# Kernel tuning notes

Measured on AMD Instinct MI355X. Metric: run time of the kernel, lower is better.

The kernel has to match this reference:

```python
import jax, jax.numpy as jnp
import numpy as np
import math

EMBED_DIM = 1024
NUM_HEADS = 16
HEAD_DIM = EMBED_DIM // NUM_HEADS
INPUT_DIM = 1024


def setup_inputs() -> dict:
    key = jax.random.key(0)
    k_x, k_wqkv, k_wout = jax.random.split(key, 3)
    x = jax.random.normal(k_x, (4, 1, 2048, INPUT_DIM), dtype=jnp.float32)
    # xavier_uniform bounds
    def xavier(k, shape):
        fan_out, fan_in = shape
        bound = math.sqrt(6.0 / (fan_in + fan_out))
        return jax.random.uniform(k, shape, jnp.float32, -bound, bound)
    w_qkv = xavier(k_wqkv, (3 * EMBED_DIM, INPUT_DIM))
    b_qkv = jnp.zeros((3 * EMBED_DIM,), jnp.float32)
    w_out = xavier(k_wout, (EMBED_DIM, EMBED_DIM))
    b_out = jnp.zeros((EMBED_DIM,), jnp.float32)
    return {"x": x, "w_qkv": w_qkv, "b_qkv": b_qkv, "w_out": w_out, "b_out": b_out}


def reference(x, w_qkv, b_qkv, w_out, b_out):
    B, y, S, _ = x.shape  # y must be 1 (module reshape constraint)
    # QKV projection: [B, y, S, 3E]
    qkv = jnp.einsum('bysd,ed->byse', x, w_qkv) + b_qkv
    # reshape to [B, S, H, 3*head_dim] then [B, H, S, 3*head_dim]
    qkv = qkv.reshape(B, S, NUM_HEADS, 3 * HEAD_DIM).transpose(0, 2, 1, 3)
    q, k, v = jnp.split(qkv, 3, axis=-1)  # each [B, H, S, head_dim]
    logits = jnp.einsum('bhqd,bhkd->bhqk', q, k) / math.sqrt(HEAD_DIM)
    attn = jax.nn.softmax(logits, axis=-1)  # [B, H, S, S]
    vals = jnp.einsum('bhqk,bhkd->bhqd', attn, v)
    vals = vals.transpose(0, 2, 1, 3).reshape(B, S, EMBED_DIM)
    return jnp.einsum('bse,oe->bso', vals, w_out) + b_out  # [B, S, E]
```

## Files before the change

### kernel.cpp

```cpp
#include <hip/hip_runtime.h>

typedef __bf16 bf16;
typedef __bf16 bf16x8 __attribute__((ext_vector_type(8)));
typedef __bf16 bf16x4 __attribute__((ext_vector_type(4)));
typedef float f32x4 __attribute__((ext_vector_type(4)));
typedef float f32x16 __attribute__((ext_vector_type(16)));
typedef unsigned int u32x4 __attribute__((ext_vector_type(4)));

#define SM_SCALE 0.18033688011f

__device__ __forceinline__ f32x4 mfma16(bf16x8 a, bf16x8 b, f32x4 c) {
    return __builtin_amdgcn_mfma_f32_16x16x32_bf16(a, b, c, 0, 0, 0);
}
__device__ __forceinline__ f32x16 mfma32(bf16x8 a, bf16x8 b, f32x16 c) {
    return __builtin_amdgcn_mfma_f32_32x32x16_bf16(a, b, c, 0, 0, 0);
}

__device__ __forceinline__ void gload_lds16(const void* g, void* l) {
    __builtin_amdgcn_global_load_lds((const __attribute__((address_space(1))) void*)g,
                                     (__attribute__((address_space(3))) void*)l,
                                     16, 0, 0);
}

__device__ __forceinline__ unsigned cvtpk_bf16(float lo, float hi) {
    unsigned r;
    asm("v_cvt_pk_bf16_f32 %0, %1, %2" : "=v"(r) : "v"(lo), "v"(hi));
    return r;
}
__device__ __forceinline__ void plane32_swap(unsigned& a, unsigned& b) {
    asm("v_permlane32_swap_b32 %0, %1" : "+v"(a), "+v"(b));
}
__device__ __forceinline__ float vexp2(float x) {
    float r;
    asm("v_exp_f32 %0, %1" : "=v"(r) : "v"(x));
    return r;
}
__device__ __forceinline__ float vrcp(float x) {
    float r;
    asm("v_rcp_f32 %0, %1" : "=v"(r) : "v"(x));
    return r;
}

__device__ __forceinline__ void vpack_store(char* VwB, unsigned vwlow, bf16x8 v0, bf16x8 v1) {
    const u32x4 a = __builtin_bit_cast(u32x4, v0);
    const u32x4 b = __builtin_bit_cast(u32x4, v1);
#pragma unroll
    for (int j = 0; j < 8; ++j) {
        const unsigned sel = (j & 1) ? 0x07060302u : 0x05040100u;
        const unsigned w = __builtin_amdgcn_perm(b[j >> 1], a[j >> 1], sel);
        *(unsigned*)(VwB + j * 128 + (vwlow ^ (unsigned)(j << 4))) = w;
    }
}

__global__ void cvt_all(const float* __restrict__ x, const float* __restrict__ wq,
                        const float* __restrict__ wo, bf16* __restrict__ xb,
                        bf16* __restrict__ wqb, bf16* __restrict__ wob) {
    constexpr int NX = (8192 * 1024) / 4, NQ = (3072 * 1024) / 4, NO = (1024 * 1024) / 4;
    const int stride = gridDim.x * blockDim.x;
    for (int i = blockIdx.x * blockDim.x + threadIdx.x; i < NX + NQ + NO; i += stride) {
        const float* src;
        bf16* dst;
        int li;
        if (i < NX)           { src = x;  dst = xb;  li = i; }
        else if (i < NX + NQ) { src = wq; dst = wqb; li = i - NX; }
        else                  { src = wo; dst = wob; li = i - NX - NQ; }
        const f32x4 v = ((const f32x4*)src)[li];
        bf16x4 o;
#pragma unroll
        for (int j = 0; j < 4; ++j) o[j] = (bf16)v[j];
        ((bf16x4*)dst)[li] = o;
    }
}

#define G_STAGE(STBUF)                                                      \
    gload_lds16(apA,             ldsA + (STBUF) * 49152);                   \
    gload_lds16(apA +  8 * 1024, ldsA + (STBUF) * 49152 + 1024);            \
    gload_lds16(apA + 16 * 1024, ldsA + (STBUF) * 49152 + 2048);            \
    gload_lds16(apA + 24 * 1024, ldsA + (STBUF) * 49152 + 3072);            \
    gload_lds16(apB,             ldsB + (STBUF) * 49152);                   \
    gload_lds16(apB +  8 * 1024, ldsB + (STBUF) * 49152 + 1024);            \
    apA += 64; apB += 64;

#define G_TILE(BUF, VM, STBUF, DOSTAGE)                                     \
  {                                                                         \
    asm volatile("s_waitcnt vmcnt(" #VM ")" ::: "memory");                  \
    __builtin_amdgcn_s_barrier();                                           \
    bf16x8 a0[4], b0[4];                                                    \
    _Pragma("unroll") for (int mf = 0; mf < 4; ++mf)                        \
      a0[mf] = *(const bf16x8*)(baseAk0 + (BUF) * 49152 + mf * 2048);       \
    _Pragma("unroll") for (int nf = 0; nf < 4; ++nf)                        \
      b0[nf] = *(const bf16x8*)(baseBk0 + (BUF) * 49152 + nf * 2048);       \
    if (DOSTAGE) { G_STAGE(STBUF) }                                         \
    __builtin_amdgcn_s_setprio(1);                                          \
    _Pragma("unroll") for (int mf = 0; mf < 4; ++mf)                        \
      _Pragma("unroll") for (int nf = 0; nf < 4; ++nf)                      \
        acc[mf][nf] = mfma16(a0[mf], b0[nf], acc[mf][nf]);                  \
    __builtin_amdgcn_s_setprio(0);                                          \
    bf16x8 a1[4], b1[4];                                                    \
    _Pragma("unroll") for (int mf = 0; mf < 4; ++mf)                        \
      a1[mf] = *(const bf16x8*)(baseAk1 + (BUF) * 49152 + mf * 2048);       \
    _Pragma("unroll") for (int nf = 0; nf < 4; ++nf)                        \
      b1[nf] = *(const bf16x8*)(baseBk1 + (BUF) * 49152 + nf * 2048);       \
    __builtin_amdgcn_s_setprio(1);                                          \
    _Pragma("unroll") for (int mf = 0; mf < 4; ++mf)                        \
      _Pragma("unroll") for (int nf = 0; nf < 4; ++nf)                      \
        acc[mf][nf] = mfma16(a1[mf], b1[nf], acc[mf][nf]);                  \
    __builtin_amdgcn_s_setprio(0);                                          \
  }

template <typename OutT, bool QSCALE>
__global__ __launch_bounds__(512) void gemm256(const bf16* __restrict__ A,
                                               const bf16* __restrict__ Bw,
                                               const float* __restrict__ bias,
                                               OutT* __restrict__ C,
                                               int M, int N, int K) {
    __shared__ char lds[3 * 49152];
    const int tid = threadIdx.x;
    const int wave = tid >> 6, lane = tid & 63;
    const int ln15 = lane & 15, g4 = lane >> 4;
    const int wr = wave >> 1, wc = wave & 1;
    const int m0 = blockIdx.x * 256, n0 = blockIdx.y * 128;

    const int srow = lane >> 3;
    const int sgsw = ((lane & 7) ^ srow) * 8;
    const bf16* apA = A  + (size_t)(m0 + wave * 32 + srow) * K + sgsw;
    const bf16* apB = Bw + (size_t)(n0 + wave * 16 + srow) * K + sgsw;
    char* const ldsA = (char*)lds + wave * 4096;
    char* const ldsB = (char*)lds + 32768 + wave * 2048;

    const int cxor = ((g4 ^ (ln15 & 7)) << 4);
    const char* baseAk0 = (const char*)lds + (wr * 64 + ln15) * 128 + cxor;
    const char* baseAk1 = (const char*)lds + (((wr * 64 + ln15) * 128 + cxor) ^ 64);
    const char* baseBk0 = (const char*)lds + 32768 + (wc * 64 + ln15) * 128 + cxor;
    const char* baseBk1 = (const char*)lds + 32768 + (((wc * 64 + ln15) * 128 + cxor) ^ 64);

    f32x4 acc[4][4] = {};

    G_STAGE(0)
    G_STAGE(1)

    for (int g = 0; g < 4; ++g) {
        G_TILE(0, 6, 2, 1)
        G_TILE(1, 6, 0, 1)
        G_TILE(2, 6, 1, 1)
    }
    G_TILE(0, 6, 2, 1)
    G_TILE(1, 6, 0, 1)
    G_TILE(2, 6, 0, 0)
    G_TILE(0, 0, 0, 0)

    float bv[4], sc[4];
#pragma unroll
    for (int nj = 0; nj < 4; ++nj) {
        const int col = n0 + wc * 64 + nj * 16 + ln15;
        bv[nj] = bias[col];
        sc[nj] = (QSCALE && (col % 192) < 64) ? SM_SCALE : 1.0f;
    }
#pragma unroll
    for (int mi = 0; mi < 4; ++mi) {
#pragma unroll
        for (int nj = 0; nj < 4; ++nj) {
            const int col = n0 + wc * 64 + nj * 16 + ln15;
#pragma unroll
            for (int i = 0; i < 4; ++i) {
                const int row = m0 + wr * 64 + mi * 16 + g4 * 4 + i;
                C[(size_t)row * N + col] = (OutT)((acc[mi][nj][i] + bv[nj]) * sc[nj]);
            }
        }
    }
}

#define ATTN_ITER(CUR, PRE)                                                          \
  {                                                                                  \
    if (PRE) {                                                                       \
      gload_lds16(kp, (char*)Ks + ((CUR ^ 1) * 8192) + wave * 1024);                 \
      gload_lds16(kp + 32 * 3072, (char*)Ks + ((CUR ^ 1) * 8192) + (4 + wave) * 1024); \
      v0 = *(const bf16x8*)vp;                                                       \
      v1 = *(const bf16x8*)(vp + 3072);                                              \
      kp += 64 * 3072;                                                               \
      vp += 64 * 3072;                                                               \
    }                                                                                \
    _Pragma("unroll") for (int kh = 0; kh < 2; ++kh) {                               \
      f32x16 s;                                                                      \
      __builtin_amdgcn_s_setprio(1);                                                 \
      s = mfma32(*(const bf16x8*)(kra[0] + CUR * 8192 + kh * 4096), qf[0], z16);     \
      _Pragma("unroll") for (int dc = 1; dc < 4; ++dc) {                             \
        const bf16x8 kf = *(const bf16x8*)(kra[dc] + CUR * 8192 + kh * 4096);        \
        s = mfma32(kf, qf[dc], s);                                                   \
      }                                                                              \
      __builtin_amdgcn_s_setprio(0);                                                 \
      unsigned pk[8];                                                                \
      _Pragma("unroll") for (int m = 0; m < 8; ++m)                                  \
        pk[m] = cvtpk_bf16(vexp2(s[2 * m]), vexp2(s[2 * m + 1]));                    \
      plane32_swap(pk[0], pk[2]);                                                    \
      plane32_swap(pk[1], pk[3]);                                                    \
      plane32_swap(pk[4], pk[6]);                                                    \
      plane32_swap(pk[5], pk[7]);                                                    \
      const bf16x8 pf0 = __builtin_bit_cast(bf16x8, (u32x4){pk[0], pk[1], pk[2], pk[3]}); \
      const bf16x8 pf1 = __builtin_bit_cast(bf16x8, (u32x4){pk[4], pk[5], pk[6], pk[7]}); \
      __builtin_amdgcn_s_setprio(1);                                                 \
      {                                                                              \
        const bf16x8 va0 = *(const bf16x8*)(VsB + CUR * 8192 + (vroff0 ^ (kh * 64)));       \
        const bf16x8 vc0 = *(const bf16x8*)(VsB + CUR * 8192 + (vroff0 ^ (kh * 64 + 32)));  \
        o0 = mfma32(pf0, va0, o0);                                                   \
        o0 = mfma32(pf1, vc0, o0);                                                   \
        const bf16x8 va1 = *(const bf16x8*)(VsB + CUR * 8192 + (vroff1 ^ (kh * 64)));       \
        const bf16x8 vc1 = *(const bf16x8*)(VsB + CUR * 8192 + (vroff1 ^ (kh * 64 + 32)));  \
        o1 = mfma32(pf0, va1, o1);                                                   \
        o1 = mfma32(pf1, vc1, o1);                                                   \
        dsumC = mfma32(pf0, ones, dsumC);                                            \
        dsumC = mfma32(pf1, ones, dsumC);                                            \
      }                                                                              \
      __builtin_amdgcn_s_setprio(0);                                                 \
    }                                                                                \
    if (PRE) vpack_store((char*)Ks + 16384 + ((CUR ^ 1) * 8192) + vd8 * 128, vwlow, v0, v1); \
    __syncthreads();                                                                 \
  }

__global__ __launch_bounds__(256) void attn_fa(const bf16* __restrict__ qkv,
                                               bf16* __restrict__ vals) {
    const int b = blockIdx.x >> 4, h = blockIdx.x & 15;
    const int q0 = blockIdx.y * 128;
    const int tid = threadIdx.x, wave = tid >> 6, lane = tid & 63;
    const int ln31 = lane & 31, hi = lane >> 5;

    __shared__ bf16 Ks[2 * 4096 + 2 * 4096];

    const size_t base = ((size_t)b * 2048) * 3072 + (size_t)h * 192;
    const bf16* Qb = qkv + base;

    bf16x8 qf[4];
    {
        const size_t qr = (size_t)(q0 + wave * 32 + ln31) * 3072;
#pragma unroll
        for (int dc = 0; dc < 4; ++dc)
            qf[dc] = *(const bf16x8*)(Qb + qr + dc * 16 + hi * 8);
    }

    const int krow0 = wave * 8 + (lane >> 3);
    const int kgsw = ((lane & 7) ^ (lane >> 3)) * 8;
    const bf16* kp = qkv + base + 64 + (size_t)krow0 * 3072 + kgsw;
    const int vr2 = tid & 31, vd8 = (tid >> 5) * 8;
    const bf16* vp = qkv + base + 128 + (size_t)(2 * vr2) * 3072 + vd8;
    const unsigned vwlow = 4u * (unsigned)vr2;

    const int kxor = (ln31 & 7) << 4;
    const char* kra[4];
#pragma unroll
    for (int dc = 0; dc < 4; ++dc)
        kra[dc] = (char*)Ks + ln31 * 128 + ((dc * 32 + hi * 16) ^ kxor);
    const char* const VsB = (char*)Ks + 16384;
    const unsigned vroff0 = (unsigned)(ln31 * 128 + ((hi * 16) ^ kxor));
    const unsigned vroff1 = vroff0 + 32 * 128;

    const bf16x8 ones = __builtin_bit_cast(bf16x8, (u32x4){0x3F803F80u, 0x3F803F80u,
                                                           0x3F803F80u, 0x3F803F80u});
    const f32x16 z16 = {};
    f32x16 o0 = {}, o1 = {}, dsumC = {};
    bf16x8 v0, v1;

    gload_lds16(kp, (char*)Ks + wave * 1024);
    gload_lds16(kp + 32 * 3072, (char*)Ks + (4 + wave) * 1024);
    v0 = *(const bf16x8*)vp;
    v1 = *(const bf16x8*)(vp + 3072);
    kp += 64 * 3072;
    vp += 64 * 3072;
    vpack_store((char*)Ks + 16384 + vd8 * 128, vwlow, v0, v1);
    __syncthreads();

    for (int tp = 0; tp < 15; ++tp) {
        ATTN_ITER(0, true)
        ATTN_ITER(1, true)
    }
    ATTN_ITER(0, true)
    ATTN_ITER(1, false)

#pragma unroll
    for (int r = 0; r < 16; ++r) {
        const float invq = vrcp(dsumC[r]);
        const int qloc = (r & 3) + 8 * (r >> 2) + 4 * hi;
        const size_t orow = ((size_t)b * 2048 + q0 + wave * 32 + qloc) * 1024 + h * 64;
        vals[orow + ln31]      = (bf16)(o0[r] * invq);
        vals[orow + 32 + ln31] = (bf16)(o1[r] * invq);
    }
}

extern "C" void kernel_launch(void* const* d_in, const int* in_sizes, int n_in,
                              void* d_out, int out_size, void* d_ws, size_t ws_size,
                              hipStream_t stream) {
    const float* x     = (const float*)d_in[0];
    const float* w_qkv = (const float*)d_in[1];
    const float* b_qkv = (const float*)d_in[2];
    const float* w_out = (const float*)d_in[3];
    const float* b_out = (const float*)d_in[4];
    float* out = (float*)d_out;

    char* ws = (char*)d_ws;
    bf16* xb   = (bf16*)ws;
    bf16* wqb  = (bf16*)(ws + (16u << 20));
    bf16* wob  = (bf16*)(ws + (22u << 20));
    bf16* qkvb = (bf16*)(ws + (24u << 20));
    bf16* valb = xb;

    cvt_all<<<dim3(2048), dim3(256), 0, stream>>>(x, w_qkv, w_out, xb, wqb, wob);

    gemm256<bf16, true><<<dim3(32, 24), dim3(512), 0, stream>>>(xb, wqb, b_qkv, qkvb,
                                                                8192, 3072, 1024);
    attn_fa<<<dim3(64, 16), dim3(256), 0, stream>>>(qkvb, valb);
    gemm256<float, false><<<dim3(32, 8), dim3(512), 0, stream>>>(valb, wob, b_out, out,
                                                                 8192, 1024, 1024);
}
```

Measured before the change: 186.7 us.

## Process two query tiles per attention block to reuse K/V LDS loads

Each attention workgroup now handles 256 query rows (two 128-row sets per wave) instead of 128, halving the grid. Every K and V tile loaded into LDS is reused for two sets of QK and PV MFMAs, which cuts global and LDS traffic per unit of work and gives each wave more independent MFMA chains to interleave. The cost is roughly doubled accumulator registers, which may lower occupancy. With 512 blocks the grid may also underfill the device's compute units.

```diff
diff --git a/kernel.cpp b/kernel.cpp
--- a/kernel.cpp
+++ b/kernel.cpp
@@ -181,37 +181,55 @@
       vp += 64 * 3072;                                                               \
     }                                                                                \
     _Pragma("unroll") for (int kh = 0; kh < 2; ++kh) {                               \
-      f32x16 s;                                                                      \
+      bf16x8 kf[4];                                                                  \
+      _Pragma("unroll") for (int dc = 0; dc < 4; ++dc)                               \
+        kf[dc] = *(const bf16x8*)(kra[dc] + CUR * 8192 + kh * 4096);                 \
+      f32x16 sA, sB;                                                                 \
       __builtin_amdgcn_s_setprio(1);                                                 \
-      s = mfma32(*(const bf16x8*)(kra[0] + CUR * 8192 + kh * 4096), qf[0], z16);     \
+      sA = mfma32(kf[0], qfA[0], z16);                                               \
+      sB = mfma32(kf[0], qfB[0], z16);                                               \
       _Pragma("unroll") for (int dc = 1; dc < 4; ++dc) {                             \
-        const bf16x8 kf = *(const bf16x8*)(kra[dc] + CUR * 8192 + kh * 4096);        \
-        s = mfma32(kf, qf[dc], s);                                                   \
+        sA = mfma32(kf[dc], qfA[dc], sA);                                            \
+        sB = mfma32(kf[dc], qfB[dc], sB);                                            \
       }                                                                              \
       __builtin_amdgcn_s_setprio(0);                                                 \
       unsigned pk[8];                                                                \
       _Pragma("unroll") for (int m = 0; m < 8; ++m)                                  \
-        pk[m] = cvtpk_bf16(vexp2(s[2 * m]), vexp2(s[2 * m + 1]));                    \
+        pk[m] = cvtpk_bf16(vexp2(sA[2 * m]), vexp2(sA[2 * m + 1]));                  \
       plane32_swap(pk[0], pk[2]);                                                    \
       plane32_swap(pk[1], pk[3]);                                                    \
       plane32_swap(pk[4], pk[6]);                                                    \
       plane32_swap(pk[5], pk[7]);                                                    \
-      const bf16x8 pf0 = __builtin_bit_cast(bf16x8, (u32x4){pk[0], pk[1], pk[2], pk[3]}); \
-      const bf16x8 pf1 = __builtin_bit_cast(bf16x8, (u32x4){pk[4], pk[5], pk[6], pk[7]}); \
-      __builtin_amdgcn_s_setprio(1);                                                 \
+      const bf16x8 pfA0 = __builtin_bit_cast(bf16x8, (u32x4){pk[0], pk[1], pk[2], pk[3]}); \
+      const bf16x8 pfA1 = __builtin_bit_cast(bf16x8, (u32x4){pk[4], pk[5], pk[6], pk[7]}); \
+      _Pragma("unroll") for (int m = 0; m < 8; ++m)                                  \
+        pk[m] = cvtpk_bf16(vexp2(sB[2 * m]), vexp2(sB[2 * m + 1]));                  \
+      plane32_swap(pk[0], pk[2]);                                                    \
+      plane32_swap(pk[1], pk[3]);                                                    \
+      plane32_swap(pk[4], pk[6]);                                                    \
+      plane32_swap(pk[5], pk[7]);                                                    \
+      const bf16x8 pfB0 = __builtin_bit_cast(bf16x8, (u32x4){pk[0], pk[1], pk[2], pk[3]}); \
+      const bf16x8 pfB1 = __builtin_bit_cast(bf16x8, (u32x4){pk[4], pk[5], pk[6], pk[7]}); \
       {                                                                              \
         const bf16x8 va0 = *(const bf16x8*)(VsB + CUR * 8192 + (vroff0 ^ (kh * 64)));       \
         const bf16x8 vc0 = *(const bf16x8*)(VsB + CUR * 8192 + (vroff0 ^ (kh * 64 + 32)));  \
-        o0 = mfma32(pf0, va0, o0);                                                   \
-        o0 = mfma32(pf1, vc0, o0);                                                   \
         const bf16x8 va1 = *(const bf16x8*)(VsB + CUR * 8192 + (vroff1 ^ (kh * 64)));       \
         const bf16x8 vc1 = *(const bf16x8*)(VsB + CUR * 8192 + (vroff1 ^ (kh * 64 + 32)));  \
-        o1 = mfma32(pf0, va1, o1);                                                   \
-        o1 = mfma32(pf1, vc1, o1);                                                   \
-        dsumC = mfma32(pf0, ones, dsumC);                                            \
-        dsumC = mfma32(pf1, ones, dsumC);                                            \
+        __builtin_amdgcn_s_setprio(1);                                               \
+        o0A = mfma32(pfA0, va0, o0A);                                                \
+        o0A = mfma32(pfA1, vc0, o0A);                                                \
+        o1A = mfma32(pfA0, va1, o1A);                                                \
+        o1A = mfma32(pfA1, vc1, o1A);                                                \
+        dsA = mfma32(pfA0, ones, dsA);                                               \
+        dsA = mfma32(pfA1, ones, dsA);                                               \
+        o0B = mfma32(pfB0, va0, o0B);                                                \
+        o0B = mfma32(pfB1, vc0, o0B);                                                \
+        o1B = mfma32(pfB0, va1, o1B);                                                \
+        o1B = mfma32(pfB1, vc1, o1B);                                                \
+        dsB = mfma32(pfB0, ones, dsB);                                               \
+        dsB = mfma32(pfB1, ones, dsB);                                               \
+        __builtin_amdgcn_s_setprio(0);                                               \
       }                                                                              \
-      __builtin_amdgcn_s_setprio(0);                                                 \
     }                                                                                \
     if (PRE) vpack_store((char*)Ks + 16384 + ((CUR ^ 1) * 8192) + vd8 * 128, vwlow, v0, v1); \
     __syncthreads();                                                                 \
@@ -220,7 +238,7 @@
 __global__ __launch_bounds__(256) void attn_fa(const bf16* __restrict__ qkv,
                                                bf16* __restrict__ vals) {
     const int b = blockIdx.x >> 4, h = blockIdx.x & 15;
-    const int q0 = blockIdx.y * 128;
+    const int q0 = blockIdx.y * 256;
     const int tid = threadIdx.x, wave = tid >> 6, lane = tid & 63;
     const int ln31 = lane & 31, hi = lane >> 5;
 
@@ -229,12 +247,15 @@
     const size_t base = ((size_t)b * 2048) * 3072 + (size_t)h * 192;
     const bf16* Qb = qkv + base;
 
-    bf16x8 qf[4];
+    bf16x8 qfA[4], qfB[4];
     {
-        const size_t qr = (size_t)(q0 + wave * 32 + ln31) * 3072;
-#pragma unroll
-        for (int dc = 0; dc < 4; ++dc)
-            qf[dc] = *(const bf16x8*)(Qb + qr + dc * 16 + hi * 8);
+        const size_t qrA = (size_t)(q0 + wave * 32 + ln31) * 3072;
+        const size_t qrB = qrA + (size_t)128 * 3072;
+#pragma unroll
+        for (int dc = 0; dc < 4; ++dc) {
+            qfA[dc] = *(const bf16x8*)(Qb + qrA + dc * 16 + hi * 8);
+            qfB[dc] = *(const bf16x8*)(Qb + qrB + dc * 16 + hi * 8);
+        }
     }
 
     const int krow0 = wave * 8 + (lane >> 3);
@@ -256,7 +277,8 @@
     const bf16x8 ones = __builtin_bit_cast(bf16x8, (u32x4){0x3F803F80u, 0x3F803F80u,
                                                            0x3F803F80u, 0x3F803F80u});
     const f32x16 z16 = {};
-    f32x16 o0 = {}, o1 = {}, dsumC = {};
+    f32x16 o0A = {}, o1A = {}, dsA = {};
+    f32x16 o0B = {}, o1B = {}, dsB = {};
     bf16x8 v0, v1;
 
     gload_lds16(kp, (char*)Ks + wave * 1024);
@@ -277,11 +299,15 @@
 
 #pragma unroll
     for (int r = 0; r < 16; ++r) {
-        const float invq = vrcp(dsumC[r]);
         const int qloc = (r & 3) + 8 * (r >> 2) + 4 * hi;
-        const size_t orow = ((size_t)b * 2048 + q0 + wave * 32 + qloc) * 1024 + h * 64;
-        vals[orow + ln31]      = (bf16)(o0[r] * invq);
-        vals[orow + 32 + ln31] = (bf16)(o1[r] * invq);
+        const size_t orowA = ((size_t)b * 2048 + q0 + wave * 32 + qloc) * 1024 + h * 64;
+        const float invA = vrcp(dsA[r]);
+        vals[orowA + ln31]      = (bf16)(o0A[r] * invA);
+        vals[orowA + 32 + ln31] = (bf16)(o1A[r] * invA);
+        const size_t orowB = orowA + (size_t)128 * 1024;
+        const float invB = vrcp(dsB[r]);
+        vals[orowB + ln31]      = (bf16)(o0B[r] * invB);
+        vals[orowB + 32 + ln31] = (bf16)(o1B[r] * invB);
     }
 }
 
@@ -306,7 +332,7 @@
 
     gemm256<bf16, true><<<dim3(32, 24), dim3(512), 0, stream>>>(xb, wqb, b_qkv, qkvb,
                                                                 8192, 3072, 1024);
-    attn_fa<<<dim3(64, 16), dim3(256), 0, stream>>>(qkvb, valb);
+    attn_fa<<<dim3(64, 8), dim3(256), 0, stream>>>(qkvb, valb);
     gemm256<float, false><<<dim3(32, 8), dim3(512), 0, stream>>>(valb, wob, b_out, out,
                                                                  8192, 1024, 1024);
 }
```

Measured after the change: 200.0 us. 7.1% more time.
